# Performance work log

Hardware: AMD Instinct MI355X
Metric: run time of the kernel (lower is better)

## Reference

```python
import jax, jax.numpy as jnp
from jax import lax
import numpy as np


def _gru_layer(X, mask, W, U, b):
    """Keras GRU (reset_after=True, gate order [z|r|h]) with Keras-style masking.

    X: [B,T,F] float, mask: [B,T] bool, W: [F,3u], U: [u,3u], b: [2,3u].
    At masked steps the state (== output for GRU) is carried over unchanged.
    Returns (outputs [B,T,u], final_state [B,u]).
    """
    B, T, _ = X.shape
    u = U.shape[0]
    # Precompute input projections for all timesteps (cuDNN-style).
    Xp = jnp.einsum('btf,fg->btg', X, W) + b[0]  # [B,T,3u]

    def step(h, inp):
        x_t, m_t = inp  # x_t: [B,3u], m_t: [B]
        rec = h @ U + b[1]  # [B,3u]
        xz, xr, xh = jnp.split(x_t, 3, axis=-1)
        rz, rr, rh = jnp.split(rec, 3, axis=-1)
        z = jax.nn.sigmoid(xz + rz)
        r = jax.nn.sigmoid(xr + rr)
        hh = jnp.tanh(xh + r * rh)
        h_new = z * h + (1.0 - z) * hh
        h_new = jnp.where(m_t[:, None], h_new, h)  # carry state at masked steps
        return h_new, h_new

    h0 = jnp.zeros((B, u), X.dtype)
    h_final, outs = lax.scan(step, h0, (jnp.swapaxes(Xp, 0, 1), mask.T))
    return jnp.swapaxes(outs, 0, 1), h_final


def setup_inputs() -> dict:
    key = jax.random.key(0)
    ks = jax.random.split(key, 12)
    B, T, F = 64, 1024, 16
    H, E = 256, 256
    vals = jax.random.randint(ks[0], (B, T, F), 0, 20, dtype=jnp.int32)
    # variable-length sequences padded with -1
    lengths = jax.random.randint(ks[1], (B,), T // 4, T + 1)
    valid = jnp.arange(T)[None, :] < lengths[:, None]
    batch = jnp.where(valid[:, :, None], vals, jnp.int32(-1))
    SCALE = 0.05

    def w(k, shape):
        return jax.random.normal(k, shape, jnp.float32) * SCALE

    return {
        'batch': batch,
        'W0': w(ks[2], (F, 3 * H)), 'U0': w(ks[3], (H, 3 * H)), 'b0': jnp.zeros((2, 3 * H), jnp.float32),
        'W1': w(ks[4], (H, 3 * H)), 'U1': w(ks[5], (H, 3 * H)), 'b1': jnp.zeros((2, 3 * H), jnp.float32),
        'W2': w(ks[6], (H, 3 * E)), 'U2': w(ks[7], (E, 3 * E)), 'b2': jnp.zeros((2, 3 * E), jnp.float32),
    }


def reference(batch, W0, U0, b0, W1, U1, b1, W2, U2, b2):
    mask = batch[:, :, -1] != -1  # [B,T]
    X = batch.astype(jnp.float32)
    X, _ = _gru_layer(X, mask, W0, U0, b0)
    X, _ = _gru_layer(X, mask, W1, U1, b1)
    out, h = _gru_layer(X, mask, W2, U2, b2)
    return out, h
```

## Files before the change

### kernel.cpp

```cpp
#include <hip/hip_runtime.h>
#include <cstdint>

#define BATCH 64
#define SEQ   1024
#define FEAT  16
#define HID   256
#define GATE  768
#define TC    64
#define LASTC 15
#define NT    512

typedef _Float16 f16x8 __attribute__((ext_vector_type(8)));
typedef float    f32x4 __attribute__((ext_vector_type(4)));

__device__ __forceinline__ float sigmoidf_(float x) { return 1.0f / (1.0f + __expf(-x)); }
__device__ __forceinline__ float tanhf_(float x)    { return 2.0f / (1.0f + __expf(-2.0f * x)) - 1.0f; }

__global__ __launch_bounds__(256) void k_packB(const float* __restrict__ U,
                                               float* __restrict__ Bfrag)
{
    const int tid = blockIdx.x * 256 + threadIdx.x;
    const int ct   = tid >> 9;
    const int kt   = (tid >> 6) & 7;
    const int lane = tid & 63;
    const int g = lane >> 4, i = lane & 15;
    const int col = ct * 16 + i;
    const int k0  = kt * 32 + g * 8;
    union { f16x8 v; float4 f; } u;
#pragma unroll
    for (int e = 0; e < 8; ++e)
        u.v[e] = (_Float16)U[(size_t)(k0 + e) * GATE + col];
    *(float4*)(Bfrag + (size_t)tid * 4) = u.f;
}

struct Params {
    const int*   batch;
    const float *W0, *b0, *b1, *b2;
    const float *Bf0, *Bf1, *Bf2;
    const float *Wp1, *Wp2;
    _Float16 *xp0a, *xp0b;
    _Float16 *xp1, *xp2;
    _Float16 *y0a, *y0b, *y1a, *y1b;
    float *h0, *h1, *h2;
    float *out, *hfin;
};

__device__ __forceinline__ void gru_body(
    char* smem, const _Float16* __restrict__ xp, const float* __restrict__ Bfrag,
    const float* __restrict__ bb, const int* __restrict__ batch,
    _Float16* __restrict__ yout, float* __restrict__ fout, int obase,
    float* __restrict__ hfinal, float* __restrict__ hstate, int t0, int b)
{
    _Float16 (*hbuf)[HID] = (_Float16 (*)[HID])smem;

    const int T  = threadIdx.x;
    const int w  = T >> 6;
    const int l  = T & 63;
    const int g  = l >> 4;
    const int i  = l & 15;
    const int g1 = g & 1;
    const int c  = 32 * w + i + 16 * g1;

    f16x8 Bf[6][8];
    {
        const int cts[6] = {2 * w, 16 + 2 * w, 32 + 2 * w,
                            2 * w + 1, 17 + 2 * w, 33 + 2 * w};
#pragma unroll
        for (int ci = 0; ci < 6; ++ci)
#pragma unroll
            for (int kt = 0; kt < 8; ++kt) {
                float4 v = *(const float4*)(Bfrag + ((size_t)(cts[ci] * 8 + kt) * 64 + l) * 4);
                Bf[ci][kt] = __builtin_bit_cast(f16x8, v);
            }
    }

    const float bh = bb[GATE + 2 * HID + c];

    float hprev = (t0 == 0) ? 0.0f : hstate[b * HID + c];
    if (l < 32) hbuf[0][32 * w + l] = (_Float16)hprev;

    _Float16 nxz, nxr, nxh; int nmf;
    {
        const _Float16* xrow = xp + ((size_t)b * TC + 0) * GATE;
        nxz = xrow[c]; nxr = xrow[HID + c]; nxh = xrow[2 * HID + c];
        nmf = batch[((size_t)b * SEQ + t0) * FEAT + (FEAT - 1)];
    }
    __syncthreads();

    for (int tl = 0; tl < TC; ++tl) {
        const _Float16 cxz = nxz, cxr = nxr, cxh = nxh;
        const int cmf = nmf;
        {
            const int tn = (tl + 1 < TC) ? tl + 1 : tl;
            const _Float16* xrow = xp + ((size_t)b * TC + tn) * GATE;
            nxz = xrow[c]; nxr = xrow[HID + c]; nxh = xrow[2 * HID + c];
            nmf = batch[((size_t)b * SEQ + t0 + tn) * FEAT + (FEAT - 1)];
        }

        const _Float16* rd = hbuf[tl & 1];

        f32x4 az0 = {0.f, 0.f, 0.f, 0.f}, ar0 = az0, ah0 = az0;
        f32x4 az1 = az0, ar1 = az0, ah1 = az0;
#pragma unroll
        for (int kt = 0; kt < 8; ++kt) {
            const f16x8 a = *(const f16x8*)(rd + kt * 32 + g * 8);
            az0 = __builtin_amdgcn_mfma_f32_16x16x32_f16(a, Bf[0][kt], az0, 0, 0, 0);
            ar0 = __builtin_amdgcn_mfma_f32_16x16x32_f16(a, Bf[1][kt], ar0, 0, 0, 0);
            ah0 = __builtin_amdgcn_mfma_f32_16x16x32_f16(a, Bf[2][kt], ah0, 0, 0, 0);
            az1 = __builtin_amdgcn_mfma_f32_16x16x32_f16(a, Bf[3][kt], az1, 0, 0, 0);
            ar1 = __builtin_amdgcn_mfma_f32_16x16x32_f16(a, Bf[4][kt], ar1, 0, 0, 0);
            ah1 = __builtin_amdgcn_mfma_f32_16x16x32_f16(a, Bf[5][kt], ah1, 0, 0, 0);
        }

        const float az = g1 ? az1[0] : az0[0];
        const float ar = g1 ? ar1[0] : ar0[0];
        const float ah = g1 ? ah1[0] : ah0[0];

        const float z  = sigmoidf_((float)cxz + az);
        const float r  = sigmoidf_((float)cxr + ar);
        const float hh = tanhf_((float)cxh + r * (ah + bh));
        float hn = z * hprev + (1.0f - z) * hh;
        hn = (cmf != -1) ? hn : hprev;
        hprev = hn;

        if (l < 32) {
            if (yout)
                yout[((size_t)b * TC + tl) * HID + 32 * w + l] = (_Float16)hn;
            else
                fout[((size_t)b * SEQ + obase + tl) * HID + 32 * w + l] = hn;
            hbuf[(tl & 1) ^ 1][32 * w + l] = (_Float16)hn;
        }
        asm volatile("s_waitcnt lgkmcnt(0)\n\ts_barrier" ::: "memory");
    }

    if (l < 32) {
        hstate[b * HID + 32 * w + l] = hprev;
        if (hfinal) hfinal[b * HID + 32 * w + l] = hprev;
    }
}

__device__ __forceinline__ void gemm_mfma_body(
    char* smem, const _Float16* __restrict__ Yc, const float* __restrict__ Wp,
    const float* __restrict__ bb, _Float16* __restrict__ xpout, int mt)
{
    _Float16 (*As)[264] = (_Float16 (*)[264])smem;

    const int T = threadIdx.x;
    const int w = T >> 6;
    const int l = T & 63;
    const int g = l >> 4;
    const int i = l & 15;

    {
        const _Float16* src = Yc + (size_t)mt * TC * HID;
#pragma unroll
        for (int q = 0; q < 4; ++q) {
            const int ch  = T * 4 + q;
            const int row = ch >> 5;
            const int ko  = (ch & 31) * 8;
            *(float4*)&As[row][ko] = *(const float4*)(src + (size_t)row * HID + ko);
        }
    }
    __syncthreads();

    f16x8 Af[4][8];
#pragma unroll
    for (int rt = 0; rt < 4; ++rt)
#pragma unroll
        for (int kt = 0; kt < 8; ++kt)
            Af[rt][kt] = *(const f16x8*)&As[rt * 16 + i][kt * 32 + g * 8];

#pragma unroll
    for (int ci = 0; ci < 6; ++ci) {
        const int ct = w * 6 + ci;
        f16x8 Bfr[8];
#pragma unroll
        for (int kt = 0; kt < 8; ++kt) {
            float4 v = *(const float4*)(Wp + ((size_t)(ct * 8 + kt) * 64 + l) * 4);
            Bfr[kt] = __builtin_bit_cast(f16x8, v);
        }
        f32x4 acc[4];
#pragma unroll
        for (int rt = 0; rt < 4; ++rt) acc[rt] = (f32x4){0.f, 0.f, 0.f, 0.f};
#pragma unroll
        for (int kt = 0; kt < 8; ++kt) {
            acc[0] = __builtin_amdgcn_mfma_f32_16x16x32_f16(Af[0][kt], Bfr[kt], acc[0], 0, 0, 0);
            acc[1] = __builtin_amdgcn_mfma_f32_16x16x32_f16(Af[1][kt], Bfr[kt], acc[1], 0, 0, 0);
            acc[2] = __builtin_amdgcn_mfma_f32_16x16x32_f16(Af[2][kt], Bfr[kt], acc[2], 0, 0, 0);
            acc[3] = __builtin_amdgcn_mfma_f32_16x16x32_f16(Af[3][kt], Bfr[kt], acc[3], 0, 0, 0);
        }
        const int n = ct * 16 + i;
        const float bias = bb[n] + ((n < 2 * HID) ? bb[GATE + n] : 0.0f);
#pragma unroll
        for (int rt = 0; rt < 4; ++rt)
#pragma unroll
            for (int r = 0; r < 4; ++r)
                xpout[(size_t)(mt * TC + rt * 16 + 4 * g + r) * GATE + n] =
                    (_Float16)(acc[rt][r] + bias);
    }
    __syncthreads();
}

__device__ __forceinline__ void xp0_body(
    char* smem, const int* __restrict__ batch, const float* __restrict__ W0,
    const float* __restrict__ bb, _Float16* __restrict__ xpout, int t0, int b)
{
    int* bl = (int*)smem;
    const int T = threadIdx.x;
    for (int idx = T; idx < TC * FEAT; idx += NT)
        bl[idx] = batch[((size_t)b * SEQ + t0 + (idx >> 4)) * FEAT + (idx & 15)];
    __syncthreads();

    const int cc0 = T;
    const int cc1 = T + NT;
    const bool two = (cc1 < GATE);

    float w0a[FEAT], w0b[FEAT];
#pragma unroll
    for (int f = 0; f < FEAT; ++f) w0a[f] = W0[f * GATE + cc0];
    if (two) {
#pragma unroll
        for (int f = 0; f < FEAT; ++f) w0b[f] = W0[f * GATE + cc1];
    }
    const float ba = bb[cc0] + ((cc0 < 2 * HID) ? bb[GATE + cc0] : 0.0f);
    const float bc = two ? (bb[cc1] + ((cc1 < 2 * HID) ? bb[GATE + cc1] : 0.0f)) : 0.0f;

    for (int tl = 0; tl < TC; ++tl) {
        float a0 = ba, a1 = bc;
#pragma unroll
        for (int f = 0; f < FEAT; ++f) {
            const float xf = (float)bl[tl * FEAT + f];
            a0 += xf * w0a[f];
            if (two) a1 += xf * w0b[f];
        }
        _Float16* orow = xpout + ((size_t)b * TC + tl) * GATE;
        orow[cc0] = (_Float16)a0;
        if (two) orow[cc1] = (_Float16)a1;
    }
    __syncthreads();
}

__global__ __launch_bounds__(NT, 1) void k_fused(Params P, int d)
{
    __shared__ __align__(16) char smem[64 * 264 * 2];
    const int bid = blockIdx.x;

    if (bid < 64) {
        const int c = d;
        if (c >= 0 && c <= LASTC)
            gru_body(smem, (c & 1) ? P.xp0b : P.xp0a, P.Bf0, P.b0, P.batch,
                     (c & 1) ? P.y0b : P.y0a, nullptr, 0, nullptr, P.h0,
                     c * TC, bid);
    } else if (bid < 128) {
        const int c = d - 1;
        const int b = bid - 64;
        if (c >= 0 && c <= LASTC) {
            gemm_mfma_body(smem, (c & 1) ? P.y0b : P.y0a, P.Wp1, P.b1, P.xp1, b);
            gru_body(smem, P.xp1, P.Bf1, P.b1, P.batch,
                     (c & 1) ? P.y1b : P.y1a, nullptr, 0, nullptr, P.h1,
                     c * TC, b);
        }
    } else if (bid < 192) {
        const int c = d - 2;
        const int b = bid - 128;
        if (c >= 0 && c <= LASTC) {
            gemm_mfma_body(smem, (c & 1) ? P.y1b : P.y1a, P.Wp2, P.b2, P.xp2, b);
            gru_body(smem, P.xp2, P.Bf2, P.b2, P.batch,
                     nullptr, P.out, c * TC, (c == LASTC) ? P.hfin : nullptr,
                     P.h2, c * TC, b);
        }
    } else {
        const int c = d + 1;
        if (c >= 0 && c <= LASTC)
            xp0_body(smem, P.batch, P.W0, P.b0,
                     (c & 1) ? P.xp0b : P.xp0a, c * TC, bid - 192);
    }
}

extern "C" void kernel_launch(void* const* d_in, const int* in_sizes, int n_in,
                              void* d_out, int out_size, void* d_ws, size_t ws_size,
                              hipStream_t stream)
{
    const int*   batch = (const int*)d_in[0];
    const float* W0 = (const float*)d_in[1];
    const float* U0 = (const float*)d_in[2];
    const float* b0 = (const float*)d_in[3];
    const float* W1 = (const float*)d_in[4];
    const float* U1 = (const float*)d_in[5];
    const float* b1 = (const float*)d_in[6];
    const float* W2 = (const float*)d_in[7];
    const float* U2 = (const float*)d_in[8];
    const float* b2 = (const float*)d_in[9];

    float* out  = (float*)d_out;
    float* hfin = out + (size_t)BATCH * SEQ * HID;

    const size_t XPB = (size_t)BATCH * TC * GATE * 2;
    const size_t YB  = (size_t)BATCH * TC * HID * 2;
    const size_t HB  = (size_t)BATCH * HID * 4;
    const size_t BFB = (size_t)48 * 8 * 64 * 4 * 4;

    char* p = (char*)d_ws;
    auto alloc = [&](size_t bytes) { char* q = p; p += (bytes + 255) & ~(size_t)255; return q; };
    _Float16* xp0a = (_Float16*)alloc(XPB);
    _Float16* xp0b = (_Float16*)alloc(XPB);
    _Float16* xp1  = (_Float16*)alloc(XPB);
    _Float16* xp2  = (_Float16*)alloc(XPB);
    _Float16* y0a  = (_Float16*)alloc(YB);
    _Float16* y0b  = (_Float16*)alloc(YB);
    _Float16* y1a  = (_Float16*)alloc(YB);
    _Float16* y1b  = (_Float16*)alloc(YB);
    float* h0  = (float*)alloc(HB);
    float* h1  = (float*)alloc(HB);
    float* h2  = (float*)alloc(HB);
    float* Bf0 = (float*)alloc(BFB);
    float* Bf1 = (float*)alloc(BFB);
    float* Bf2 = (float*)alloc(BFB);
    float* Wp1 = (float*)alloc(BFB);
    float* Wp2 = (float*)alloc(BFB);

    dim3 gpack(48 * 8 * 64 / 256), bpack(256);
    k_packB<<<gpack, bpack, 0, stream>>>(U0, Bf0);
    k_packB<<<gpack, bpack, 0, stream>>>(U1, Bf1);
    k_packB<<<gpack, bpack, 0, stream>>>(U2, Bf2);
    k_packB<<<gpack, bpack, 0, stream>>>(W1, Wp1);
    k_packB<<<gpack, bpack, 0, stream>>>(W2, Wp2);

    Params P;
    P.batch = batch;
    P.W0 = W0; P.b0 = b0; P.b1 = b1; P.b2 = b2;
    P.Bf0 = Bf0; P.Bf1 = Bf1; P.Bf2 = Bf2;
    P.Wp1 = Wp1; P.Wp2 = Wp2;
    P.xp0a = xp0a; P.xp0b = xp0b;
    P.xp1 = xp1; P.xp2 = xp2;
    P.y0a = y0a; P.y0b = y0b; P.y1a = y1a; P.y1b = y1b;
    P.h0 = h0; P.h1 = h1; P.h2 = h2;
    P.out = out; P.hfin = hfin;

    for (int d = -1; d <= LASTC + 2; ++d)
        k_fused<<<dim3(256), dim3(NT), 0, stream>>>(P, d);
}
```

Baseline: 1.382 ms.

## Keep per-chunk input projections in LDS instead of global workspace

Input projections for each GRU chunk are now computed straight into a padded LDS buffer (about 131 KB of shared memory per block), and the recurrent loop reads them from LDS. The layer-0 projection moves into the layer-0 GRU block instead of running in separate blocks a step ahead, which drops 64 blocks and one launch. Step masks are also precomputed into LDS as bytes. This removes global writes and reads of the projection buffers and per-step global loads on the serial path, but adds the layer-0 projection to the critical path of each chunk.

```diff
diff --git a/kernel.cpp b/kernel.cpp
--- a/kernel.cpp
+++ b/kernel.cpp
@@ -10,6 +10,13 @@
 #define LASTC 15
 #define NT    512
 
+#define XPLD  776
+#define XP_OFF 0
+#define HB_OFF 99328
+#define MK_OFF 100352
+#define AS_OFF 100416
+#define SMEM_SZ 134208
+
 typedef _Float16 f16x8 __attribute__((ext_vector_type(8)));
 typedef float    f32x4 __attribute__((ext_vector_type(4)));
 
@@ -38,20 +45,20 @@
     const float *W0, *b0, *b1, *b2;
     const float *Bf0, *Bf1, *Bf2;
     const float *Wp1, *Wp2;
-    _Float16 *xp0a, *xp0b;
-    _Float16 *xp1, *xp2;
     _Float16 *y0a, *y0b, *y1a, *y1b;
     float *h0, *h1, *h2;
     float *out, *hfin;
 };
 
 __device__ __forceinline__ void gru_body(
-    char* smem, const _Float16* __restrict__ xp, const float* __restrict__ Bfrag,
+    char* smem, const float* __restrict__ Bfrag,
     const float* __restrict__ bb, const int* __restrict__ batch,
     _Float16* __restrict__ yout, float* __restrict__ fout, int obase,
     float* __restrict__ hfinal, float* __restrict__ hstate, int t0, int b)
 {
-    _Float16 (*hbuf)[HID] = (_Float16 (*)[HID])smem;
+    const _Float16* xpL = (const _Float16*)(smem + XP_OFF);
+    _Float16 (*hbuf)[HID] = (_Float16 (*)[HID])(smem + HB_OFF);
+    unsigned char* mkl = (unsigned char*)(smem + MK_OFF);
 
     const int T  = threadIdx.x;
     const int w  = T >> 6;
@@ -76,26 +83,18 @@
 
     const float bh = bb[GATE + 2 * HID + c];
 
+    for (int idx = T; idx < TC; idx += NT)
+        mkl[idx] = (unsigned char)(batch[((size_t)b * SEQ + t0 + idx) * FEAT + (FEAT - 1)] != -1);
+
     float hprev = (t0 == 0) ? 0.0f : hstate[b * HID + c];
     if (l < 32) hbuf[0][32 * w + l] = (_Float16)hprev;
-
-    _Float16 nxz, nxr, nxh; int nmf;
-    {
-        const _Float16* xrow = xp + ((size_t)b * TC + 0) * GATE;
-        nxz = xrow[c]; nxr = xrow[HID + c]; nxh = xrow[2 * HID + c];
-        nmf = batch[((size_t)b * SEQ + t0) * FEAT + (FEAT - 1)];
-    }
     __syncthreads();
 
     for (int tl = 0; tl < TC; ++tl) {
-        const _Float16 cxz = nxz, cxr = nxr, cxh = nxh;
-        const int cmf = nmf;
-        {
-            const int tn = (tl + 1 < TC) ? tl + 1 : tl;
-            const _Float16* xrow = xp + ((size_t)b * TC + tn) * GATE;
-            nxz = xrow[c]; nxr = xrow[HID + c]; nxh = xrow[2 * HID + c];
-            nmf = batch[((size_t)b * SEQ + t0 + tn) * FEAT + (FEAT - 1)];
-        }
+        const _Float16 cxz = xpL[tl * XPLD + c];
+        const _Float16 cxr = xpL[tl * XPLD + HID + c];
+        const _Float16 cxh = xpL[tl * XPLD + 2 * HID + c];
+        const int cmf = mkl[tl];
 
         const _Float16* rd = hbuf[tl & 1];
 
@@ -120,7 +119,7 @@
         const float r  = sigmoidf_((float)cxr + ar);
         const float hh = tanhf_((float)cxh + r * (ah + bh));
         float hn = z * hprev + (1.0f - z) * hh;
-        hn = (cmf != -1) ? hn : hprev;
+        hn = cmf ? hn : hprev;
         hprev = hn;
 
         if (l < 32) {
@@ -139,11 +138,12 @@
     }
 }
 
-__device__ __forceinline__ void gemm_mfma_body(
+__device__ __forceinline__ void gemm_mfma_lds(
     char* smem, const _Float16* __restrict__ Yc, const float* __restrict__ Wp,
-    const float* __restrict__ bb, _Float16* __restrict__ xpout, int mt)
-{
-    _Float16 (*As)[264] = (_Float16 (*)[264])smem;
+    const float* __restrict__ bb, int mt)
+{
+    _Float16 (*As)[264] = (_Float16 (*)[264])(smem + AS_OFF);
+    _Float16* xpL = (_Float16*)(smem + XP_OFF);
 
     const int T = threadIdx.x;
     const int w = T >> 6;
@@ -195,17 +195,16 @@
         for (int rt = 0; rt < 4; ++rt)
 #pragma unroll
             for (int r = 0; r < 4; ++r)
-                xpout[(size_t)(mt * TC + rt * 16 + 4 * g + r) * GATE + n] =
-                    (_Float16)(acc[rt][r] + bias);
-    }
-    __syncthreads();
-}
-
-__device__ __forceinline__ void xp0_body(
+                xpL[(rt * 16 + 4 * g + r) * XPLD + n] = (_Float16)(acc[rt][r] + bias);
+    }
+}
+
+__device__ __forceinline__ void xp0_lds(
     char* smem, const int* __restrict__ batch, const float* __restrict__ W0,
-    const float* __restrict__ bb, _Float16* __restrict__ xpout, int t0, int b)
-{
-    int* bl = (int*)smem;
+    const float* __restrict__ bb, int t0, int b)
+{
+    int* bl = (int*)(smem + AS_OFF);
+    _Float16* xpL = (_Float16*)(smem + XP_OFF);
     const int T = threadIdx.x;
     for (int idx = T; idx < TC * FEAT; idx += NT)
         bl[idx] = batch[((size_t)b * SEQ + t0 + (idx >> 4)) * FEAT + (idx & 15)];
@@ -233,47 +232,43 @@
             a0 += xf * w0a[f];
             if (two) a1 += xf * w0b[f];
         }
-        _Float16* orow = xpout + ((size_t)b * TC + tl) * GATE;
-        orow[cc0] = (_Float16)a0;
-        if (two) orow[cc1] = (_Float16)a1;
-    }
-    __syncthreads();
+        xpL[tl * XPLD + cc0] = (_Float16)a0;
+        if (two) xpL[tl * XPLD + cc1] = (_Float16)a1;
+    }
 }
 
 __global__ __launch_bounds__(NT, 1) void k_fused(Params P, int d)
 {
-    __shared__ __align__(16) char smem[64 * 264 * 2];
+    __shared__ __align__(16) char smem[SMEM_SZ];
     const int bid = blockIdx.x;
 
     if (bid < 64) {
         const int c = d;
-        if (c >= 0 && c <= LASTC)
-            gru_body(smem, (c & 1) ? P.xp0b : P.xp0a, P.Bf0, P.b0, P.batch,
+        const int b = bid;
+        if (c >= 0 && c <= LASTC) {
+            xp0_lds(smem, P.batch, P.W0, P.b0, c * TC, b);
+            gru_body(smem, P.Bf0, P.b0, P.batch,
                      (c & 1) ? P.y0b : P.y0a, nullptr, 0, nullptr, P.h0,
-                     c * TC, bid);
+                     c * TC, b);
+        }
     } else if (bid < 128) {
         const int c = d - 1;
         const int b = bid - 64;
         if (c >= 0 && c <= LASTC) {
-            gemm_mfma_body(smem, (c & 1) ? P.y0b : P.y0a, P.Wp1, P.b1, P.xp1, b);
-            gru_body(smem, P.xp1, P.Bf1, P.b1, P.batch,
+            gemm_mfma_lds(smem, (c & 1) ? P.y0b : P.y0a, P.Wp1, P.b1, b);
+            gru_body(smem, P.Bf1, P.b1, P.batch,
                      (c & 1) ? P.y1b : P.y1a, nullptr, 0, nullptr, P.h1,
                      c * TC, b);
         }
-    } else if (bid < 192) {
+    } else {
         const int c = d - 2;
         const int b = bid - 128;
         if (c >= 0 && c <= LASTC) {
-            gemm_mfma_body(smem, (c & 1) ? P.y1b : P.y1a, P.Wp2, P.b2, P.xp2, b);
-            gru_body(smem, P.xp2, P.Bf2, P.b2, P.batch,
+            gemm_mfma_lds(smem, (c & 1) ? P.y1b : P.y1a, P.Wp2, P.b2, b);
+            gru_body(smem, P.Bf2, P.b2, P.batch,
                      nullptr, P.out, c * TC, (c == LASTC) ? P.hfin : nullptr,
                      P.h2, c * TC, b);
         }
-    } else {
-        const int c = d + 1;
-        if (c >= 0 && c <= LASTC)
-            xp0_body(smem, P.batch, P.W0, P.b0,
-                     (c & 1) ? P.xp0b : P.xp0a, c * TC, bid - 192);
     }
 }
 
@@ -295,17 +290,12 @@
     float* out  = (float*)d_out;
     float* hfin = out + (size_t)BATCH * SEQ * HID;
 
-    const size_t XPB = (size_t)BATCH * TC * GATE * 2;
     const size_t YB  = (size_t)BATCH * TC * HID * 2;
     const size_t HB  = (size_t)BATCH * HID * 4;
     const size_t BFB = (size_t)48 * 8 * 64 * 4 * 4;
 
     char* p = (char*)d_ws;
     auto alloc = [&](size_t bytes) { char* q = p; p += (bytes + 255) & ~(size_t)255; return q; };
-    _Float16* xp0a = (_Float16*)alloc(XPB);
-    _Float16* xp0b = (_Float16*)alloc(XPB);
-    _Float16* xp1  = (_Float16*)alloc(XPB);
-    _Float16* xp2  = (_Float16*)alloc(XPB);
     _Float16* y0a  = (_Float16*)alloc(YB);
     _Float16* y0b  = (_Float16*)alloc(YB);
     _Float16* y1a  = (_Float16*)alloc(YB);
@@ -331,12 +321,10 @@
     P.W0 = W0; P.b0 = b0; P.b1 = b1; P.b2 = b2;
     P.Bf0 = Bf0; P.Bf1 = Bf1; P.Bf2 = Bf2;
     P.Wp1 = Wp1; P.Wp2 = Wp2;
-    P.xp0a = xp0a; P.xp0b = xp0b;
-    P.xp1 = xp1; P.xp2 = xp2;
     P.y0a = y0a; P.y0b = y0b; P.y1a = y1a; P.y1b = y1b;
     P.h0 = h0; P.h1 = h1; P.h2 = h2;
     P.out = out; P.hfin = hfin;
 
-    for (int d = -1; d <= LASTC + 2; ++d)
-        k_fused<<<dim3(256), dim3(NT), 0, stream>>>(P, d);
-}
+    for (int d = 0; d <= LASTC + 2; ++d)
+        k_fused<<<dim3(192), dim3(NT), 0, stream>>>(P, d);
+}
```

Measured after the change: 1.463 ms. 5.9% more time.
